# Kernel tuning notes

Hardware: AMD Instinct MI355X
Metric: run time of the kernel (lower is better)

## Reference

```python
import jax, jax.numpy as jnp
import numpy as np

BN_EPS = 1e-5

def conv1x1(x, w, b):
    # x: [N,C,T,V], w: [O,C], b: [O]
    return jnp.einsum('nctv,oc->notv', x, w) + b[None, :, None, None]

def conv9(x, w, b):
    # (9,1) temporal conv, padding (4,0). x: [N,C,T,V], w: [O,C,9], b: [O]
    out = jax.lax.conv_general_dilated(
        x, w[:, :, :, None], window_strides=(1, 1), padding=((4, 4), (0, 0)),
        dimension_numbers=('NCHW', 'OIHW', 'NCHW'))
    return out + b[None, :, None, None]

def attn_adj(f1, f2):
    # f1,f2: [N,inter,T,V] -> softmax over rows (axis -2) of [N,V,V]
    N, ic, T, V = f1.shape
    a1 = jnp.transpose(f1, (0, 3, 1, 2)).reshape(N, V, ic * T)  # permute(0,3,1,2).view
    a2 = f2.reshape(N, ic * T, V)
    scores = jnp.einsum('nvk,nkw->nvw', a1, a2) / (ic * T)
    return jax.nn.softmax(scores, axis=-2)


def setup_inputs() -> dict:
    key = jax.random.key(0)
    ks = jax.random.split(key, 16)
    N, C, T, V, S, IC = 16, 256, 64, 25, 3, 64
    s = lambda k, shape, sc=0.05: jax.random.normal(k, shape, dtype=jnp.float32) * sc
    return {
        'x': jax.random.normal(ks[0], (N, C, T, V), dtype=jnp.float32),
        'A': jax.random.uniform(ks[1], (S, V, V), dtype=jnp.float32),
        'PA': s(ks[2], (S, V, V), 1e-3),
        'wa': s(ks[3], (S, IC, C)), 'ba': jnp.zeros((S, IC), jnp.float32),
        'wb': s(ks[4], (S, IC, C)), 'bb': jnp.zeros((S, IC), jnp.float32),
        'wT1': s(ks[5], (S, IC, C, 9)), 'bT1': jnp.zeros((S, IC), jnp.float32),
        'wT2': s(ks[6], (S, IC, C, 9)), 'bT2': jnp.zeros((S, IC), jnp.float32),
        'wST11': s(ks[7], (S, IC, C, 9)), 'bST11': jnp.zeros((S, IC), jnp.float32),
        'wST12': s(ks[8], (S, IC, C, 9)), 'bST12': jnp.zeros((S, IC), jnp.float32),
        'wd': s(ks[9], (S, C, C)), 'bd': jnp.zeros((S, C), jnp.float32),
        'gamma': jnp.ones((C,), jnp.float32), 'beta': jnp.zeros((C,), jnp.float32),
        'bn_mean': jnp.zeros((C,), jnp.float32), 'bn_var': jnp.ones((C,), jnp.float32),
    }


def reference(x, A, PA, wa, ba, wb, bb, wT1, bT1, wT2, bT2,
              wST11, bST11, wST12, bST12, wd, bd, gamma, beta, bn_mean, bn_var):
    N, C, T, V = x.shape
    I = jnp.eye(V, dtype=x.dtype)
    # Chebyshev-like static graph transforms (computed once in __init__ in torch)
    A_ch4s = jax.nn.softmax((8 * A**4 - 4 * A**2 - 4 * A + I) / V, axis=-2)
    A_ch3 = 4 * A**2 - A - 2 * I
    A_all = A_ch3 + A_ch4s + PA  # [3,V,V]

    xf = x.reshape(N, C * T, V)
    y = 0.0
    for i in range(3):
        A1 = attn_adj(conv1x1(x, wa[i], ba[i]), conv1x1(x, wb[i], bb[i]))
        AT = attn_adj(conv9(x, wT1[i], bT1[i]), conv9(x, wT2[i], bT2[i]))
        # ModuleList append quirk: even i -> 1x1 conv (center tap), odd i -> (9,1) conv
        if i % 2 == 0:
            s1 = conv1x1(x, wST11[i, :, :, 4], bST11[i])
            s2 = conv1x1(x, wST12[i, :, :, 4], bST12[i])
        else:
            s1 = conv9(x, wST11[i], bST11[i])
            s2 = conv9(x, wST12[i], bST12[i])
        AST = attn_adj(s1, s2)
        Ai = A_all[i] + A1 + AT + AST  # [N,V,V]
        z = jnp.einsum('nkv,nvw->nkw', xf, Ai).reshape(N, C, T, V)
        y = y + conv1x1(z, wd[i], bd[i])

    yb = (y - bn_mean[None, :, None, None]) * (gamma[None, :, None, None]
         / jnp.sqrt(bn_var[None, :, None, None] + BN_EPS)) + beta[None, :, None, None]
    return jax.nn.relu(yb + x)  # down is identity (in_channels == out_channels)
```

## Files before the change

kernel.cpp:

```cpp
#include <hip/hip_runtime.h>
#include <hip/hip_bf16.h>

#define NN 16
#define CC 256
#define TT 64
#define VV 25
#define ICC 64
#define TV 1600
#define CTV 409600
#define NICTV 1638400

typedef __bf16 v8bf __attribute__((ext_vector_type(8)));
typedef __bf16 v4bf __attribute__((ext_vector_type(4)));
typedef float f32x16 __attribute__((ext_vector_type(16)));

struct ConvPairs {
  const __bf16* wA[5];
  const __bf16* wB[5];
  const float*  bA[5];
  const float*  bB[5];
};

__global__ __launch_bounds__(256) void prep_k(
    const float* __restrict__ x, __bf16* __restrict__ xt,
    const float* __restrict__ wT1, const float* __restrict__ wT2,
    const float* __restrict__ wST11, const float* __restrict__ wST12,
    __bf16* __restrict__ wT1b,
    __bf16* __restrict__ wS1c, __bf16* __restrict__ wS2c,
    const float* __restrict__ wa, const float* __restrict__ wb,
    __bf16* __restrict__ wab,
    const float* __restrict__ wd, __bf16* __restrict__ wdb,
    const float* __restrict__ A, const float* __restrict__ PA,
    float* __restrict__ Aall){
  __shared__ float smf[64*65];
  int b = blockIdx.x;
  int tid = threadIdx.x;
  if (b < 768){
    int r = b & 191, t = b >> 8;
    r = b % 192; t = b / 192;
    const float* in = (t==0)?wT1:(t==1)?wT2:(t==2)?wST11:wST12;
    for (int i = tid; i < 2304; i += 256) smf[i] = in[(size_t)r*2304 + i];
    __syncthreads();
    __bf16* ob = wT1b + (size_t)t*442368 + (size_t)r*2304;
    for (int i = tid; i < 2304; i += 256){
      int k = i >> 8, c = i & 255;
      ob[i] = (__bf16)smf[c*9 + k];
    }
  } else if (b < 960){
    int i = (b-768)*256 + tid;
    if (i < 49152){
      wS1c[i] = (__bf16)wST11[i*9 + 4];
      wS2c[i] = (__bf16)wST12[i*9 + 4];
    }
  } else if (b < 1344){
    int i = (b-960)*256 + tid;
    if (i < 2*49152)
      wab[i] = (__bf16)((i < 49152) ? wa[i] : wb[i - 49152]);
  } else if (b < 2112){
    int i = (b-1344)*256 + tid;
    if (i < 196608) wdb[i] = (__bf16)wd[i];
  } else if (b == 2112){
    int t = tid;
    if (t < 75){
      int s = t / 25, w = t % 25;
      float a[25], m[25];
      float mx = -3.4e38f;
      for (int v = 0; v < 25; ++v){
        float av = A[(s*25 + v)*25 + w];
        a[v] = av;
        float d = (v == w) ? 1.f : 0.f;
        float mm = (8.f*av*av*av*av - 4.f*av*av - 4.f*av + d) * 0.04f;
        m[v] = mm;
        mx = fmaxf(mx, mm);
      }
      float sum = 0.f;
      for (int v = 0; v < 25; ++v){ float e = __expf(m[v]-mx); m[v] = e; sum += e; }
      float inv = 1.f/sum;
      for (int v = 0; v < 25; ++v){
        float av = a[v];
        float d = (v == w) ? 1.f : 0.f;
        Aall[(s*25+v)*25 + w] = m[v]*inv + 4.f*av*av - av - 2.f*d + PA[(s*25+v)*25+w];
      }
    }
  } else {
    int idx = b - 2113;
    int p0 = (idx % 25)*64, c0 = ((idx/25) & 3)*64, n = idx/100;
    for (int i = tid; i < 4096; i += 256){
      int cc = i >> 6, pp = i & 63;
      smf[cc*65+pp] = x[(size_t)n*CTV + (size_t)(c0+cc)*TV + p0 + pp];
    }
    __syncthreads();
    for (int i = tid; i < 4096; i += 256){
      int pp = i >> 6, cc = i & 63;
      xt[((size_t)n*TV + p0+pp)*256 + c0+cc] = (__bf16)smf[cc*65+pp];
    }
  }
}

template<int NTAPS, int CW, int WSTRIDE>
__global__ __launch_bounds__(256, 2) void conv6_k(const __bf16* __restrict__ xt,
    ConvPairs cp, __bf16* __restrict__ fbuf){
  extern __shared__ __bf16 sm[];
  constexpr int HALO  = (NTAPS==9) ? 100 : 0;
  constexpr int NROWS = 256 + 2*HALO;
  constexpr int GPR   = CW/8;
  constexpr int NCH   = 256/CW;
  constexpr int KS    = CW/16;
  constexpr int NSTEP = NTAPS*KS;
  int p0 = blockIdx.x*256;
  int n  = blockIdx.y;
  int pr = blockIdx.z;
  int tid = threadIdx.x;
  int lane = tid & 63;
  int wave = tid >> 6;
  int which = wave >> 1, ph = wave & 1;
  int h = lane >> 5, l31 = lane & 31;
  const __bf16* wgt = which ? cp.wB[pr] : cp.wA[pr];
  const float* bias = which ? cp.bB[pr] : cp.bA[pr];
  const __bf16* xtn = xt + (size_t)n*CTV;
  const __bf16* wl = wgt + (size_t)l31*WSTRIDE + h*8;

  f32x16 acc[2][4];
  #pragma unroll
  for (int a=0;a<2;++a)
    #pragma unroll
    for (int b=0;b<4;++b)
      #pragma unroll
      for (int r=0;r<16;++r) acc[a][b][r] = 0.f;

  int rowbase = ph*128 + l31;

  for (int ch=0; ch<NCH; ++ch){
    for (int s2 = tid; s2 < NROWS*GPR; s2 += 256){
      int row = s2 / GPR, g = s2 % GPR;
      int pg = p0 - HALO + row;
      uint4 val = make_uint4(0u,0u,0u,0u);
      if ((unsigned)pg < 1600u)
        val = *(const uint4*)(xtn + (size_t)pg*256 + ch*CW + g*8);
      int gs = (g + row) & (GPR-1);
      *(uint4*)(sm + row*CW + gs*8) = val;
    }
    __syncthreads();
    const __bf16* wc = wl + ch*CW;
    auto ldA = [&](int s, v8bf& A0, v8bf& A1){
      int tap = s / KS, ks = s % KS;
      const __bf16* p = wc + (size_t)tap*256 + ks*16;
      A0 = *(const v8bf*)(p);
      A1 = *(const v8bf*)(p + (size_t)32*WSTRIDE);
    };
    auto ldB = [&](int s, v8bf* bb){
      int tap = s / KS, ks = s % KS;
      int rowb = (NTAPS==9 ? tap*25 : 0) + rowbase;
      #pragma unroll
      for (int pq=0; pq<4; ++pq){
        int row = rowb + pq*32;
        int gs = ((ks*2 + h) + row) & (GPR-1);
        bb[pq] = *(const v8bf*)(sm + row*CW + gs*8);
      }
    };
    v8bf a0[4], a1[4];
    ldA(0, a0[0], a1[0]);
    ldA(1, a0[1], a1[1]);
    ldA(2, a0[2], a1[2]);
    ldA(3, a0[3], a1[3]);
    v8bf bc[4], bn[4];
    ldB(0, bc);
    #pragma unroll
    for (int s=0; s<NSTEP; ++s){
      if (s+1 < NSTEP) ldB(s+1, bn);
      int cur = s & 3;
      v8bf A0 = a0[cur], A1 = a1[cur];
      if (s+4 < NSTEP) ldA(s+4, a0[cur], a1[cur]);
      #pragma unroll
      for (int pq=0; pq<4; ++pq){
        acc[0][pq] = __builtin_amdgcn_mfma_f32_32x32x16_bf16(A0, bc[pq], acc[0][pq], 0,0,0);
        acc[1][pq] = __builtin_amdgcn_mfma_f32_32x32x16_bf16(A1, bc[pq], acc[1][pq], 0,0,0);
      }
      #pragma unroll
      for (int pq=0; pq<4; ++pq) bc[pq] = bn[pq];
    }
    __syncthreads();
  }

  __bf16* outb = fbuf + (size_t)(pr*2 + which)*NICTV + (size_t)n*TV*64;
  #pragma unroll
  for (int pq=0; pq<4; ++pq){
    int p = p0 + ph*128 + pq*32 + l31;
    if (p >= 1600) continue;
    __bf16* orow = outb + (size_t)p*64;
    #pragma unroll
    for (int oq=0; oq<2; ++oq){
      #pragma unroll
      for (int g=0; g<4; ++g){
        int og = oq*32 + 8*g + 4*h;
        v4bf pk;
        #pragma unroll
        for (int j=0;j<4;++j) pk[j] = (__bf16)(acc[oq][pq][4*g+j] + bias[og+j]);
        *(v4bf*)(orow + og) = pk;
      }
    }
  }
}

__global__ __launch_bounds__(256, 2) void ugemm5_k(const __bf16* __restrict__ xt,
    const __bf16* __restrict__ wdb, __bf16* __restrict__ ubuf){
  extern __shared__ __bf16 sm[];
  int p0 = blockIdx.x*128;
  int n  = blockIdx.y;
  int br = blockIdx.z;
  int tid = threadIdx.x;
  int lane = tid & 63;
  int os = tid >> 6;
  int h = lane >> 5, l31 = lane & 31;
  const __bf16* xtn = xt + (size_t)n*CTV;

  f32x16 acc[2][4];
  #pragma unroll
  for (int a=0;a<2;++a)
    #pragma unroll
    for (int b=0;b<4;++b)
      #pragma unroll
      for (int r=0;r<16;++r) acc[a][b][r] = 0.f;

  for (int s2 = tid; s2 < 128*32; s2 += 256){
    int row = s2 >> 5, g = s2 & 31;
    int pg = p0 + row;
    uint4 val = make_uint4(0u,0u,0u,0u);
    if (pg < 1600)
      val = *(const uint4*)(xtn + (size_t)pg*256 + g*8);
    int gs = (g + row) & 31;
    *(uint4*)(sm + row*256 + gs*8) = val;
  }
  __syncthreads();

  const __bf16* wl = wdb + ((size_t)br*256 + os*64 + l31)*256 + h*8;
  auto ldA = [&](int ks, v8bf& A0, v8bf& A1){
    A0 = *(const v8bf*)(wl + ks*16);
    A1 = *(const v8bf*)(wl + (size_t)32*256 + ks*16);
  };
  auto ldB = [&](int ks, v8bf* bb){
    #pragma unroll
    for (int pq=0; pq<4; ++pq){
      int row = pq*32 + l31;
      int gs = ((ks*2 + h) + row) & 31;
      bb[pq] = *(const v8bf*)(sm + row*256 + gs*8);
    }
  };
  v8bf a0[4], a1[4];
  ldA(0, a0[0], a1[0]);
  ldA(1, a0[1], a1[1]);
  ldA(2, a0[2], a1[2]);
  ldA(3, a0[3], a1[3]);
  v8bf bc[4], bn[4];
  ldB(0, bc);
  #pragma unroll
  for (int ks=0; ks<16; ++ks){
    if (ks+1 < 16) ldB(ks+1, bn);
    int cur = ks & 3;
    v8bf A0 = a0[cur], A1 = a1[cur];
    if (ks+4 < 16) ldA(ks+4, a0[cur], a1[cur]);
    #pragma unroll
    for (int pq=0; pq<4; ++pq){
      acc[0][pq] = __builtin_amdgcn_mfma_f32_32x32x16_bf16(A0, bc[pq], acc[0][pq], 0,0,0);
      acc[1][pq] = __builtin_amdgcn_mfma_f32_32x32x16_bf16(A1, bc[pq], acc[1][pq], 0,0,0);
    }
    #pragma unroll
    for (int pq=0; pq<4; ++pq) bc[pq] = bn[pq];
  }

  #pragma unroll
  for (int pq=0; pq<4; ++pq){
    int p = p0 + pq*32 + l31;
    if (p >= 1600) continue;
    __bf16* out = ubuf + ((size_t)(br*NN + n)*TV + p)*256;
    #pragma unroll
    for (int oq=0; oq<2; ++oq){
      #pragma unroll
      for (int g=0; g<4; ++g){
        int og = os*64 + oq*32 + 8*g + 4*h;
        v4bf pk;
        #pragma unroll
        for (int j=0;j<4;++j) pk[j] = (__bf16)acc[oq][pq][4*g+j];
        *(v4bf*)(out + og) = pk;
      }
    }
  }
}

__global__ __launch_bounds__(256) void scores_m_k(const __bf16* __restrict__ fbuf,
                                                  float* __restrict__ part, int pairbase){
  int n = blockIdx.y, pr = blockIdx.z;
  int tid = threadIdx.x;
  int lane = tid & 63;
  int wave = tid >> 6;
  int chunk = blockIdx.x*4 + wave;
  int h = lane >> 5, l31 = lane & 31;
  const __bf16* f1 = fbuf + (size_t)(pr*2)*NICTV   + (size_t)n*TV*64;
  const __bf16* f2 = fbuf + (size_t)(pr*2+1)*NICTV + (size_t)n*TV*64;
  int t0 = chunk*4;

  f32x16 acc;
  #pragma unroll
  for (int r=0;r<16;++r) acc[r] = 0.f;

  auto off = [&](int s)->size_t{
    int t = t0 + (s>>2), og = s&3;
    return ((size_t)(t*25 + l31))*64 + og*16 + h*8;
  };
  v8bf A[2], B[2];
  { size_t o0 = off(0); A[0] = *(const v8bf*)(f1+o0); B[0] = *(const v8bf*)(f2+o0); }
  { size_t o1 = off(1); A[1] = *(const v8bf*)(f1+o1); B[1] = *(const v8bf*)(f2+o1); }
  #pragma unroll
  for (int s=0; s<16; ++s){
    int cur = s & 1;
    v8bf Ac = A[cur], Bc = B[cur];
    if (s+2 < 16){
      size_t o2 = off(s+2);
      A[cur] = *(const v8bf*)(f1+o2);
      B[cur] = *(const v8bf*)(f2+o2);
    }
    acc = __builtin_amdgcn_mfma_f32_32x32x16_bf16(Ac, Bc, acc, 0,0,0);
  }

  size_t tile = (((size_t)(pairbase+pr)*NN + n)*16 + chunk);
  float* pt = part + tile*1024;
  #pragma unroll
  for (int r=0; r<16; ++r){
    int row = (r&3) + 8*(r>>2) + 4*h;
    pt[row*32 + l31] = acc[r];
  }
}

__global__ __launch_bounds__(64) void reduce_all_k(const float* __restrict__ part,
    const float* __restrict__ Aall, float* __restrict__ Ai3){
  const int pairbr[9] = {0,1,2,0,2, 0,1,2,1};
  int n = blockIdx.x, w = blockIdx.y;
  int lane = threadIdx.x;
  float accbr[3] = {0.f, 0.f, 0.f};
  for (int pr=0; pr<9; ++pr){
    float s = 0.f;
    if (lane < 25){
      const float* pp = part + (((size_t)pr*NN + n)*16)*1024 + lane*32 + w;
      #pragma unroll
      for (int ch=0; ch<16; ++ch) s += pp[(size_t)ch*1024];
    }
    s *= (1.f/4096.f);
    float mval = (lane<25) ? s : -3.4e38f;
    #pragma unroll
    for (int d=32; d>0; d>>=1) mval = fmaxf(mval, __shfl_xor(mval, d));
    float e = (lane<25) ? __expf(s - mval) : 0.f;
    float sum = e;
    #pragma unroll
    for (int d=32; d>0; d>>=1) sum += __shfl_xor(sum, d);
    accbr[pairbr[pr]] += e / sum;
  }
  if (lane < 25){
    #pragma unroll
    for (int br=0; br<3; ++br)
      Ai3[((size_t)br*NN + n)*625 + lane*25 + w] =
        Aall[br*625 + lane*25 + w] + accbr[br];
  }
}

__global__ __launch_bounds__(256) void yep_k(const float* __restrict__ x,
    const float* __restrict__ Ai3, const __bf16* __restrict__ ubuf,
    const float* __restrict__ bd, const float* __restrict__ gamma,
    const float* __restrict__ beta, const float* __restrict__ bnm,
    const float* __restrict__ bnv, float* __restrict__ out){
  __shared__ float ais[3][25*28];
  int t = blockIdx.x, n = blockIdx.y, o = threadIdx.x;
  for (int l=o; l<2100; l+=256){
    int br = l/700, r = l%700;
    int v = r/28, w = r%28;
    ais[br][v*28+w] = (w<25) ? Ai3[((size_t)br*NN + n)*625 + v*25 + w] : 0.f;
  }
  __syncthreads();
  float y[28];
  #pragma unroll
  for (int w=0;w<28;++w) y[w]=0.f;
  for (int br=0; br<3; ++br){
    const __bf16* up = ubuf + ((size_t)(br*NN + n)*TV + t*25)*256 + o;
    float uv[25];
    #pragma unroll
    for (int v=0;v<25;++v) uv[v] = (float)up[(size_t)v*256];
    const float* ab = ais[br];
    for (int v=0; v<25; ++v){
      float u = uv[v];
      #pragma unroll
      for (int j=0; j<7; ++j){
        float4 a4 = *(const float4*)(ab + v*28 + 4*j);
        y[4*j+0] = fmaf(u, a4.x, y[4*j+0]);
        y[4*j+1] = fmaf(u, a4.y, y[4*j+1]);
        y[4*j+2] = fmaf(u, a4.z, y[4*j+2]);
        y[4*j+3] = fmaf(u, a4.w, y[4*j+3]);
      }
    }
  }
  float bsum = bd[o] + bd[256+o] + bd[512+o];
  float sc = gamma[o] * rsqrtf(bnv[o] + 1e-5f);
  float m  = bnm[o], be = beta[o];
  const float* xr = x + (size_t)n*CTV + (size_t)o*TV + t*25;
  float* orow = out + (size_t)n*CTV + (size_t)o*TV + t*25;
  #pragma unroll
  for (int w=0; w<25; ++w)
    orow[w] = fmaxf((y[w] + bsum - m)*sc + be + xr[w], 0.f);
}

extern "C" void kernel_launch(void* const* d_in, const int* in_sizes, int n_in,
                              void* d_out, int out_size, void* d_ws, size_t ws_size,
                              hipStream_t stream) {
  const float* x     = (const float*)d_in[0];
  const float* A     = (const float*)d_in[1];
  const float* PA    = (const float*)d_in[2];
  const float* wa    = (const float*)d_in[3];
  const float* ba    = (const float*)d_in[4];
  const float* wb    = (const float*)d_in[5];
  const float* bb    = (const float*)d_in[6];
  const float* wT1   = (const float*)d_in[7];
  const float* bT1   = (const float*)d_in[8];
  const float* wT2   = (const float*)d_in[9];
  const float* bT2   = (const float*)d_in[10];
  const float* wST11 = (const float*)d_in[11];
  const float* bST11 = (const float*)d_in[12];
  const float* wST12 = (const float*)d_in[13];
  const float* bST12 = (const float*)d_in[14];
  const float* wd    = (const float*)d_in[15];
  const float* bd    = (const float*)d_in[16];
  const float* gamma = (const float*)d_in[17];
  const float* beta  = (const float*)d_in[18];
  const float* bnm   = (const float*)d_in[19];
  const float* bnv   = (const float*)d_in[20];

  char* W = (char*)d_ws;
  float*  Aall = (float*)W;  W += 8192;
  float*  Ai3  = (float*)W;  W += 122880;
  __bf16* wab  = (__bf16*)W; W += 98304;
  __bf16* wbb  = (__bf16*)W; W += 98304;
  __bf16* wT1b = (__bf16*)W; W += 884736;
  __bf16* wT2b = (__bf16*)W; W += 884736;
  __bf16* wS1b = (__bf16*)W; W += 884736;
  __bf16* wS2b = (__bf16*)W; W += 884736;
  __bf16* wS1c = (__bf16*)W; W += 98304;
  __bf16* wS2c = (__bf16*)W; W += 98304;
  __bf16* wdb  = (__bf16*)W; W += 393216;
  __bf16* xt   = (__bf16*)W; W += 13107200;
  char* R = W;               W += 39321600;
  float*  part = (float*)W;  W += 9437184;
  __bf16* fbuf = (__bf16*)R;
  __bf16* ubuf = (__bf16*)R;

  prep_k<<<3713, 256, 0, stream>>>(x, xt, wT1, wT2, wST11, wST12, wT1b,
                                   wS1c, wS2c, wa, wb, wab, wd, wdb, A, PA, Aall);

  {
    ConvPairs cp;
    for (int i=0;i<3;++i){
      cp.wA[i] = wab + i*16384;  cp.wB[i] = wbb + i*16384;
      cp.bA[i] = ba + i*64;      cp.bB[i] = bb + i*64;
    }
    int evens[2] = {0, 2};
    for (int j=0;j<2;++j){
      int i = evens[j];
      cp.wA[3+j] = wS1c + i*16384;  cp.wB[3+j] = wS2c + i*16384;
      cp.bA[3+j] = bST11 + i*64;    cp.bB[3+j] = bST12 + i*64;
    }
    conv6_k<1,128,256><<<dim3(7,16,5), 256, 256*128*2, stream>>>(xt, cp, fbuf);
    scores_m_k<<<dim3(4,16,5), 256, 0, stream>>>(fbuf, part, 0);
  }

  {
    ConvPairs cp;
    for (int i=0;i<3;++i){
      cp.wA[i] = wT1b + i*147456;  cp.wB[i] = wT2b + i*147456;
      cp.bA[i] = bT1 + i*64;       cp.bB[i] = bT2 + i*64;
    }
    cp.wA[3] = wS1b + 1*147456;  cp.wB[3] = wS2b + 1*147456;
    cp.bA[3] = bST11 + 1*64;     cp.bB[3] = bST12 + 1*64;
    cp.wA[4] = cp.wA[3]; cp.wB[4] = cp.wB[3]; cp.bA[4] = cp.bA[3]; cp.bB[4] = cp.bB[3];
    conv6_k<9,64,2304><<<dim3(7,16,4), 256, 456*64*2, stream>>>(xt, cp, fbuf);
    scores_m_k<<<dim3(4,16,4), 256, 0, stream>>>(fbuf, part, 5);
  }

  ugemm5_k<<<dim3(13,16,3), 256, 128*256*2, stream>>>(xt, wdb, ubuf);
  reduce_all_k<<<dim3(16,25), 64, 0, stream>>>(part, Aall, Ai3);
  yep_k<<<dim3(64,16), 256, 0, stream>>>(x, Ai3, ubuf, bd, gamma, beta, bnm, bnv,
                                         (float*)d_out);
}
```

Measured before the change: 362.3 us.

## Pre-pack conv weights in MFMA fragment order and retile waves over outputs

Result: no change. 357.0 us (-1.5%).

```diff
diff --git a/kernel.cpp b/kernel.cpp
--- a/kernel.cpp
+++ b/kernel.cpp
@@ -25,41 +25,65 @@
     const float* __restrict__ x, __bf16* __restrict__ xt,
     const float* __restrict__ wT1, const float* __restrict__ wT2,
     const float* __restrict__ wST11, const float* __restrict__ wST12,
-    __bf16* __restrict__ wT1b,
-    __bf16* __restrict__ wS1c, __bf16* __restrict__ wS2c,
+    __bf16* __restrict__ wT1p, __bf16* __restrict__ wT2p,
+    __bf16* __restrict__ wS1p, __bf16* __restrict__ wS2p,
     const float* __restrict__ wa, const float* __restrict__ wb,
-    __bf16* __restrict__ wab,
+    __bf16* __restrict__ wabp, __bf16* __restrict__ wScp,
     const float* __restrict__ wd, __bf16* __restrict__ wdb,
     const float* __restrict__ A, const float* __restrict__ PA,
     float* __restrict__ Aall){
-  __shared__ float smf[64*65];
+  __shared__ __align__(16) float smf[64*65];
+  __bf16* smb = (__bf16*)smf;
   int b = blockIdx.x;
   int tid = threadIdx.x;
-  if (b < 768){
-    int r = b & 191, t = b >> 8;
-    r = b % 192; t = b / 192;
-    const float* in = (t==0)?wT1:(t==1)?wT2:(t==2)?wST11:wST12;
-    for (int i = tid; i < 2304; i += 256) smf[i] = in[(size_t)r*2304 + i];
+  if (b < 64){
+    int t = b >> 3, ch = (b >> 1) & 3, o2 = b & 1;
+    const float* src; __bf16* dst;
+    if (t < 3)      { src = wT1  + (size_t)t*147456;     dst = wT1p + (size_t)t*147456; }
+    else if (t < 6) { src = wT2  + (size_t)(t-3)*147456; dst = wT2p + (size_t)(t-3)*147456; }
+    else if (t == 6){ src = wST11 + 147456;              dst = wS1p; }
+    else            { src = wST12 + 147456;              dst = wS2p; }
+    const float* in = src + (size_t)(o2*32)*2304 + ch*576;
+    for (int i = tid; i < 32*576; i += 256){
+      int row = i / 576, cc = i % 576;
+      smb[i] = (__bf16)in[(size_t)row*2304 + cc];
+    }
     __syncthreads();
-    __bf16* ob = wT1b + (size_t)t*442368 + (size_t)r*2304;
-    for (int i = tid; i < 2304; i += 256){
-      int k = i >> 8, c = i & 255;
-      ob[i] = (__bf16)smf[c*9 + k];
-    }
-  } else if (b < 960){
-    int i = (b-768)*256 + tid;
-    if (i < 49152){
-      wS1c[i] = (__bf16)wST11[i*9 + 4];
-      wS2c[i] = (__bf16)wST12[i*9 + 4];
-    }
-  } else if (b < 1344){
-    int i = (b-960)*256 + tid;
-    if (i < 2*49152)
-      wab[i] = (__bf16)((i < 49152) ? wa[i] : wb[i - 49152]);
-  } else if (b < 2112){
-    int i = (b-1344)*256 + tid;
+    for (int i = tid; i < 18432; i += 256){
+      int e = i & 7, l = (i >> 3) & 63, ks = (i >> 9) & 3, tap = i >> 11;
+      int ol = l & 31, hh = l >> 5;
+      int cl = ks*16 + hh*8 + e;
+      dst[(size_t)((((ch*9 + tap)*4 + ks)*2 + o2)*512) + l*8 + e]
+          = smb[ol*576 + cl*9 + tap];
+    }
+  } else if (b < 74){
+    int u = b - 64;
+    for (int it = 0; it < 8; ++it){
+      int idx = tid + it*256;
+      int l = idx & 63, o2 = (idx >> 6) & 1, ks = (idx >> 7) & 7, ch = idx >> 10;
+      int o = o2*32 + (l & 31), hh = l >> 5;
+      int cb = ch*128 + ks*16 + hh*8;
+      __bf16 v[8];
+      if (u < 6){
+        const float* w = (u < 3) ? (wa + (size_t)u*16384) : (wb + (size_t)(u-3)*16384);
+        const float* p = w + (size_t)o*256 + cb;
+        #pragma unroll
+        for (int e = 0; e < 8; ++e) v[e] = (__bf16)p[e];
+      } else {
+        int i9 = ((u == 6) || (u == 8)) ? 0 : 2;
+        const float* w = ((u < 8) ? wST11 : wST12) + (size_t)i9*147456;
+        const float* p = w + ((size_t)o*256 + cb)*9 + 4;
+        #pragma unroll
+        for (int e = 0; e < 8; ++e) v[e] = (__bf16)p[(size_t)e*9];
+      }
+      __bf16* dst = (u < 6) ? (wabp + (size_t)u*16384) : (wScp + (size_t)(u-6)*16384);
+      #pragma unroll
+      for (int e = 0; e < 8; ++e) dst[(size_t)idx*8 + e] = v[e];
+    }
+  } else if (b < 842){
+    int i = (b-74)*256 + tid;
     if (i < 196608) wdb[i] = (__bf16)wd[i];
-  } else if (b == 2112){
+  } else if (b == 842){
     int t = tid;
     if (t < 75){
       int s = t / 25, w = t % 25;
@@ -83,7 +107,7 @@
       }
     }
   } else {
-    int idx = b - 2113;
+    int idx = b - 843;
     int p0 = (idx % 25)*64, c0 = ((idx/25) & 3)*64, n = idx/100;
     for (int i = tid; i < 4096; i += 256){
       int cc = i >> 6, pp = i & 63;
@@ -97,8 +121,8 @@
   }
 }
 
-template<int NTAPS, int CW, int WSTRIDE>
-__global__ __launch_bounds__(256, 2) void conv6_k(const __bf16* __restrict__ xt,
+template<int NTAPS, int CW>
+__global__ __launch_bounds__(256, 2) void conv7_k(const __bf16* __restrict__ xt,
     ConvPairs cp, __bf16* __restrict__ fbuf){
   extern __shared__ __bf16 sm[];
   constexpr int HALO  = (NTAPS==9) ? 100 : 0;
@@ -112,23 +136,21 @@
   int pr = blockIdx.z;
   int tid = threadIdx.x;
   int lane = tid & 63;
-  int wave = tid >> 6;
-  int which = wave >> 1, ph = wave & 1;
+  int wq = tid >> 6;
   int h = lane >> 5, l31 = lane & 31;
-  const __bf16* wgt = which ? cp.wB[pr] : cp.wA[pr];
-  const float* bias = which ? cp.bB[pr] : cp.bA[pr];
+  const __bf16* wpA = cp.wA[pr] + lane*8;
+  const __bf16* wpB = cp.wB[pr] + lane*8;
   const __bf16* xtn = xt + (size_t)n*CTV;
-  const __bf16* wl = wgt + (size_t)l31*WSTRIDE + h*8;
-
-  f32x16 acc[2][4];
-  #pragma unroll
-  for (int a=0;a<2;++a)
-    #pragma unroll
-    for (int b=0;b<4;++b)
+
+  f32x16 acc[4][2];
+  #pragma unroll
+  for (int a=0;a<4;++a)
+    #pragma unroll
+    for (int b=0;b<2;++b)
       #pragma unroll
       for (int r=0;r<16;++r) acc[a][b][r] = 0.f;
 
-  int rowbase = ph*128 + l31;
+  int rowbase = wq*64 + l31;
 
   for (int ch=0; ch<NCH; ++ch){
     for (int s2 = tid; s2 < NROWS*GPR; s2 += 256){
@@ -141,61 +163,63 @@
       *(uint4*)(sm + row*CW + gs*8) = val;
     }
     __syncthreads();
-    const __bf16* wc = wl + ch*CW;
-    auto ldA = [&](int s, v8bf& A0, v8bf& A1){
+    auto ldA = [&](int s, v8bf* aa){
       int tap = s / KS, ks = s % KS;
-      const __bf16* p = wc + (size_t)tap*256 + ks*16;
-      A0 = *(const v8bf*)(p);
-      A1 = *(const v8bf*)(p + (size_t)32*WSTRIDE);
+      size_t o = (size_t)((ch*NTAPS + tap)*KS + ks)*1024;
+      aa[0] = *(const v8bf*)(wpA + o);
+      aa[1] = *(const v8bf*)(wpA + o + 512);
+      aa[2] = *(const v8bf*)(wpB + o);
+      aa[3] = *(const v8bf*)(wpB + o + 512);
     };
     auto ldB = [&](int s, v8bf* bb){
       int tap = s / KS, ks = s % KS;
       int rowb = (NTAPS==9 ? tap*25 : 0) + rowbase;
       #pragma unroll
-      for (int pq=0; pq<4; ++pq){
+      for (int pq=0; pq<2; ++pq){
         int row = rowb + pq*32;
         int gs = ((ks*2 + h) + row) & (GPR-1);
         bb[pq] = *(const v8bf*)(sm + row*CW + gs*8);
       }
     };
-    v8bf a0[4], a1[4];
-    ldA(0, a0[0], a1[0]);
-    ldA(1, a0[1], a1[1]);
-    ldA(2, a0[2], a1[2]);
-    ldA(3, a0[3], a1[3]);
-    v8bf bc[4], bn[4];
+    v8bf ar[2][4];
+    ldA(0, ar[0]);
+    ldA(1, ar[1]);
+    v8bf bc[2], bn[2];
     ldB(0, bc);
     #pragma unroll
     for (int s=0; s<NSTEP; ++s){
       if (s+1 < NSTEP) ldB(s+1, bn);
-      int cur = s & 3;
-      v8bf A0 = a0[cur], A1 = a1[cur];
-      if (s+4 < NSTEP) ldA(s+4, a0[cur], a1[cur]);
-      #pragma unroll
-      for (int pq=0; pq<4; ++pq){
+      int cur = s & 1;
+      v8bf A0 = ar[cur][0], A1 = ar[cur][1], A2 = ar[cur][2], A3 = ar[cur][3];
+      if (s+2 < NSTEP) ldA(s+2, ar[cur]);
+      #pragma unroll
+      for (int pq=0; pq<2; ++pq){
         acc[0][pq] = __builtin_amdgcn_mfma_f32_32x32x16_bf16(A0, bc[pq], acc[0][pq], 0,0,0);
         acc[1][pq] = __builtin_amdgcn_mfma_f32_32x32x16_bf16(A1, bc[pq], acc[1][pq], 0,0,0);
-      }
-      #pragma unroll
-      for (int pq=0; pq<4; ++pq) bc[pq] = bn[pq];
+        acc[2][pq] = __builtin_amdgcn_mfma_f32_32x32x16_bf16(A2, bc[pq], acc[2][pq], 0,0,0);
+        acc[3][pq] = __builtin_amdgcn_mfma_f32_32x32x16_bf16(A3, bc[pq], acc[3][pq], 0,0,0);
+      }
+      bc[0] = bn[0]; bc[1] = bn[1];
     }
     __syncthreads();
   }
 
-  __bf16* outb = fbuf + (size_t)(pr*2 + which)*NICTV + (size_t)n*TV*64;
-  #pragma unroll
-  for (int pq=0; pq<4; ++pq){
-    int p = p0 + ph*128 + pq*32 + l31;
-    if (p >= 1600) continue;
-    __bf16* orow = outb + (size_t)p*64;
-    #pragma unroll
-    for (int oq=0; oq<2; ++oq){
+  #pragma unroll
+  for (int f=0; f<4; ++f){
+    int which = f >> 1, o2 = f & 1;
+    const float* bias = which ? cp.bB[pr] : cp.bA[pr];
+    __bf16* outb = fbuf + (size_t)(pr*2 + which)*NICTV + (size_t)n*TV*64;
+    #pragma unroll
+    for (int pq=0; pq<2; ++pq){
+      int p = p0 + wq*64 + pq*32 + l31;
+      if (p >= 1600) continue;
+      __bf16* orow = outb + (size_t)p*64;
       #pragma unroll
       for (int g=0; g<4; ++g){
-        int og = oq*32 + 8*g + 4*h;
+        int og = o2*32 + 8*g + 4*h;
         v4bf pk;
         #pragma unroll
-        for (int j=0;j<4;++j) pk[j] = (__bf16)(acc[oq][pq][4*g+j] + bias[og+j]);
+        for (int j=0;j<4;++j) pk[j] = (__bf16)(acc[f][pq][4*g+j] + bias[og+j]);
         *(v4bf*)(orow + og) = pk;
       }
     }
@@ -434,14 +458,12 @@
   char* W = (char*)d_ws;
   float*  Aall = (float*)W;  W += 8192;
   float*  Ai3  = (float*)W;  W += 122880;
-  __bf16* wab  = (__bf16*)W; W += 98304;
-  __bf16* wbb  = (__bf16*)W; W += 98304;
-  __bf16* wT1b = (__bf16*)W; W += 884736;
-  __bf16* wT2b = (__bf16*)W; W += 884736;
-  __bf16* wS1b = (__bf16*)W; W += 884736;
-  __bf16* wS2b = (__bf16*)W; W += 884736;
-  __bf16* wS1c = (__bf16*)W; W += 98304;
-  __bf16* wS2c = (__bf16*)W; W += 98304;
+  __bf16* wabp = (__bf16*)W; W += 196608;
+  __bf16* wScp = (__bf16*)W; W += 131072;
+  __bf16* wT1p = (__bf16*)W; W += 884736;
+  __bf16* wT2p = (__bf16*)W; W += 884736;
+  __bf16* wS1p = (__bf16*)W; W += 294912;
+  __bf16* wS2p = (__bf16*)W; W += 294912;
   __bf16* wdb  = (__bf16*)W; W += 393216;
   __bf16* xt   = (__bf16*)W; W += 13107200;
   char* R = W;               W += 39321600;
@@ -449,35 +471,36 @@
   __bf16* fbuf = (__bf16*)R;
   __bf16* ubuf = (__bf16*)R;
 
-  prep_k<<<3713, 256, 0, stream>>>(x, xt, wT1, wT2, wST11, wST12, wT1b,
-                                   wS1c, wS2c, wa, wb, wab, wd, wdb, A, PA, Aall);
+  prep_k<<<2443, 256, 0, stream>>>(x, xt, wT1, wT2, wST11, wST12,
+                                   wT1p, wT2p, wS1p, wS2p,
+                                   wa, wb, wabp, wScp, wd, wdb, A, PA, Aall);
 
   {
     ConvPairs cp;
     for (int i=0;i<3;++i){
-      cp.wA[i] = wab + i*16384;  cp.wB[i] = wbb + i*16384;
-      cp.bA[i] = ba + i*64;      cp.bB[i] = bb + i*64;
+      cp.wA[i] = wabp + (size_t)i*16384;      cp.wB[i] = wabp + (size_t)(3+i)*16384;
+      cp.bA[i] = ba + i*64;                   cp.bB[i] = bb + i*64;
     }
     int evens[2] = {0, 2};
     for (int j=0;j<2;++j){
       int i = evens[j];
-      cp.wA[3+j] = wS1c + i*16384;  cp.wB[3+j] = wS2c + i*16384;
-      cp.bA[3+j] = bST11 + i*64;    cp.bB[3+j] = bST12 + i*64;
-    }
-    conv6_k<1,128,256><<<dim3(7,16,5), 256, 256*128*2, stream>>>(xt, cp, fbuf);
+      cp.wA[3+j] = wScp + (size_t)j*16384;    cp.wB[3+j] = wScp + (size_t)(2+j)*16384;
+      cp.bA[3+j] = bST11 + i*64;              cp.bB[3+j] = bST12 + i*64;
+    }
+    conv7_k<1,128><<<dim3(7,16,5), 256, 256*128*2, stream>>>(xt, cp, fbuf);
     scores_m_k<<<dim3(4,16,5), 256, 0, stream>>>(fbuf, part, 0);
   }
 
   {
     ConvPairs cp;
     for (int i=0;i<3;++i){
-      cp.wA[i] = wT1b + i*147456;  cp.wB[i] = wT2b + i*147456;
-      cp.bA[i] = bT1 + i*64;       cp.bB[i] = bT2 + i*64;
-    }
-    cp.wA[3] = wS1b + 1*147456;  cp.wB[3] = wS2b + 1*147456;
-    cp.bA[3] = bST11 + 1*64;     cp.bB[3] = bST12 + 1*64;
+      cp.wA[i] = wT1p + (size_t)i*147456;  cp.wB[i] = wT2p + (size_t)i*147456;
+      cp.bA[i] = bT1 + i*64;               cp.bB[i] = bT2 + i*64;
+    }
+    cp.wA[3] = wS1p;  cp.wB[3] = wS2p;
+    cp.bA[3] = bST11 + 64;  cp.bB[3] = bST12 + 64;
     cp.wA[4] = cp.wA[3]; cp.wB[4] = cp.wB[3]; cp.bA[4] = cp.bA[3]; cp.bB[4] = cp.bB[3];
-    conv6_k<9,64,2304><<<dim3(7,16,4), 256, 456*64*2, stream>>>(xt, cp, fbuf);
+    conv7_k<9,64><<<dim3(7,16,4), 256, 456*64*2, stream>>>(xt, cp, fbuf);
     scores_m_k<<<dim3(4,16,4), 256, 0, stream>>>(fbuf, part, 5);
   }
 
```
